# Performance work log

Hardware: AMD Instinct MI355X
Metric: run time of the kernel (lower is better)

Reference implementation:

```python
import jax, jax.numpy as jnp
import numpy as np

B, S, D = 1, 2048, 2048
H, KVH, HD = 32, 8, 64
FFN = 8192
N_EXPERTS, TOP_K = 32, 4
EPS = 1e-5
NEG = -1e9


def setup_inputs() -> dict:
    key = jax.random.key(0)
    ks = jax.random.split(key, 24)
    s = 0.02
    inp = {}
    inp['hidden_states'] = jax.random.normal(ks[0], (B, S, D), jnp.float32)
    # RoPE tables: cos/sin of shape [B, S, HD]
    inv_freq = 1.0 / (10000.0 ** (np.arange(0, HD, 2, dtype=np.float32) / HD))
    t = np.arange(S, dtype=np.float32)
    freqs = np.outer(t, inv_freq)                      # [S, HD/2]
    emb = np.concatenate([freqs, freqs], axis=-1)      # [S, HD]
    inp['cos'] = jnp.asarray(np.cos(emb))[None].repeat(B, axis=0)
    inp['sin'] = jnp.asarray(np.sin(emb))[None].repeat(B, axis=0)
    # additive causal mask [B, 1, S, S]
    causal = jnp.where(jnp.tril(jnp.ones((S, S), bool)), 0.0, NEG).astype(jnp.float32)
    inp['attention_mask'] = jnp.broadcast_to(causal[None, None], (B, 1, S, S))
    # attention params
    inp['wq'] = jax.random.normal(ks[1], (H * HD, D), jnp.float32) * s
    inp['bq'] = jnp.zeros((H * HD,), jnp.float32)
    inp['wk'] = jax.random.normal(ks[2], (KVH * HD, D), jnp.float32) * s
    inp['bk'] = jnp.zeros((KVH * HD,), jnp.float32)
    inp['wv'] = jax.random.normal(ks[3], (KVH * HD, D), jnp.float32) * s
    inp['bv'] = jnp.zeros((KVH * HD,), jnp.float32)
    inp['wo'] = jax.random.normal(ks[4], (D, H * HD), jnp.float32) * s
    inp['bo'] = jnp.zeros((D,), jnp.float32)
    # norms
    inp['ln1_w'] = jnp.ones((D,), jnp.float32)
    inp['ln2_w'] = jnp.ones((D,), jnp.float32)
    # MoE gate + shared expert MLP
    inp['gate_w'] = jax.random.normal(ks[5], (N_EXPERTS, D), jnp.float32) * s
    inp['gate_b'] = jnp.zeros((N_EXPERTS,), jnp.float32)
    inp['w1'] = jax.random.normal(ks[6], (FFN, D), jnp.float32) * s
    inp['b1'] = jnp.zeros((FFN,), jnp.float32)
    inp['w2'] = jax.random.normal(ks[7], (D, FFN), jnp.float32) * s
    inp['b2'] = jnp.zeros((D,), jnp.float32)
    inp['w3'] = jax.random.normal(ks[8], (FFN, D), jnp.float32) * s
    inp['b3'] = jnp.zeros((FFN,), jnp.float32)
    return inp


def _rms_norm(x, w, eps=EPS):
    x32 = x.astype(jnp.float32)
    var = jnp.mean(x32 * x32, axis=-1, keepdims=True)
    return (w * (x32 * jax.lax.rsqrt(var + eps))).astype(x.dtype)


def _rotate_half(x):
    x1, x2 = jnp.split(x, 2, axis=-1)
    return jnp.concatenate([-x2, x1], axis=-1)


def _decoder_layer(hidden_states, cos, sin, attention_mask,
                   wq, bq, wk, bk, wv, bv, wo, bo, ln1_w, ln2_w,
                   gate_w, gate_b, w1, b1, w2, b2, w3, b3):
    residual = hidden_states
    x = _rms_norm(hidden_states, ln1_w)

    # projections -> [B, heads, S, HD]
    q = (x @ wq.T + bq).reshape(B, S, H, HD).transpose(0, 2, 1, 3)
    k = (x @ wk.T + bk).reshape(B, S, KVH, HD).transpose(0, 2, 1, 3)
    v = (x @ wv.T + bv).reshape(B, S, KVH, HD).transpose(0, 2, 1, 3)

    # RoPE (cos/sin unsqueezed on head dim)
    c, s_ = cos[:, None], sin[:, None]
    q = q * c + _rotate_half(q) * s_
    k = k * c + _rotate_half(k) * s_

    # GQA: repeat kv heads
    n_rep = H // KVH
    k = jnp.repeat(k, n_rep, axis=1)
    v = jnp.repeat(v, n_rep, axis=1)

    scaling = HD ** -0.5
    scores = jnp.einsum('bhqd,bhkd->bhqk', q, k) * scaling + attention_mask
    probs = jax.nn.softmax(scores.astype(jnp.float32), axis=-1).astype(q.dtype)
    attn = jnp.einsum('bhqk,bhkd->bhqd', probs, v)
    attn = attn.transpose(0, 2, 1, 3).reshape(B, S, H * HD)
    attn = attn @ wo.T + bo

    hidden_states = residual + attn
    residual = hidden_states
    x = _rms_norm(hidden_states, ln2_w)

    # MoE block (as written in source: router computed, but ALL tokens go
    # through one shared expert MLP; routing weights unused in output)
    flat = x.reshape(-1, D)
    router_logits = flat @ gate_w.T + gate_b                     # [B*S, E]
    rw = jax.nn.softmax(router_logits.astype(jnp.float32), axis=-1)
    rw_top, sel = jax.lax.top_k(rw, TOP_K)                       # computed, unused
    del rw_top, sel

    h1 = flat @ w1.T + b1
    h3 = flat @ w3.T + b3
    mlp = (jax.nn.silu(h1) * h3) @ w2.T + b2
    hidden_states = residual + mlp.reshape(B, S, D)
    return hidden_states


def reference(hidden_states, cos, sin, attention_mask,
              wq, bq, wk, bk, wv, bv, wo, bo, ln1_w, ln2_w,
              gate_w, gate_b, w1, b1, w2, b2, w3, b3):
    return _decoder_layer(hidden_states, cos, sin, attention_mask,
                          wq, bq, wk, bk, wv, bv, wo, bo, ln1_w, ln2_w,
                          gate_w, gate_b, w1, b1, w2, b2, w3, b3)
```

## Files before the change

kernel.cpp:

```cpp
#include <hip/hip_runtime.h>

#define S_LEN 2048
#define DMODEL 2048
#define NH 32
#define NKV 8
#define HD 64
#define FFN_DIM 8192

typedef __attribute__((ext_vector_type(4))) float f32x4;
typedef __attribute__((ext_vector_type(16))) float f32x16;
typedef __attribute__((ext_vector_type(8))) short bf16x8;

#define MFMA(a, b, c) __builtin_amdgcn_mfma_f32_16x16x32_bf16(a, b, c, 0, 0, 0)
#define MFMA32(a, b, c) __builtin_amdgcn_mfma_f32_32x32x16_bf16(a, b, c, 0, 0, 0)

__device__ __forceinline__ ushort f2bf(float f) {
  unsigned u = __float_as_uint(f);
  unsigned r = (u + 0x7fffu + ((u >> 16) & 1u)) >> 16;
  return (ushort)r;
}
__device__ __forceinline__ float bf2f(ushort s) {
  return __uint_as_float(((unsigned)s) << 16);
}
__device__ __forceinline__ unsigned cvtpk(float a, float b) {
  unsigned r;
  asm("v_cvt_pk_bf16_f32 %0, %1, %2" : "=v"(r) : "v"(a), "v"(b));
  return r;
}

__device__ __forceinline__ void gload16(const void* g, void* l) {
  __builtin_amdgcn_global_load_lds(
      (const __attribute__((address_space(1))) void*)g,
      (__attribute__((address_space(3))) void*)l, 16, 0, 0);
}

__device__ __forceinline__ void cvt_row8(const float* src, ushort* dst,
                                         int i) {
  f32x4 a = *(const f32x4*)(src + i);
  f32x4 b = *(const f32x4*)(src + i + 4);
  bf16x8 r;
#pragma unroll
  for (int j = 0; j < 4; j++) r[j] = (short)f2bf(a[j]);
#pragma unroll
  for (int j = 0; j < 4; j++) r[4 + j] = (short)f2bf(b[j]);
  *(bf16x8*)(dst + i) = r;
}

__global__ __launch_bounds__(256) void pre_k(
    const float* __restrict__ hidden, const float* __restrict__ ln1,
    ushort* __restrict__ x1, const float* __restrict__ wq,
    const float* __restrict__ wk, const float* __restrict__ wv,
    ushort* __restrict__ cw, const float* __restrict__ bq,
    const float* __restrict__ bk, const float* __restrict__ bv,
    float* __restrict__ bqkv) {
  const int b = blockIdx.x;
  const int tid = threadIdx.x;
  if (b < 2048) {
    const float* x = hidden + (size_t)b * DMODEL;
    f32x4 v0 = *(const f32x4*)(x + tid * 8);
    f32x4 v1 = *(const f32x4*)(x + tid * 8 + 4);
    float ss = v0[0] * v0[0] + v0[1] * v0[1] + v0[2] * v0[2] + v0[3] * v0[3] +
               v1[0] * v1[0] + v1[1] * v1[1] + v1[2] * v1[2] + v1[3] * v1[3];
#pragma unroll
    for (int off = 32; off; off >>= 1) ss += __shfl_xor(ss, off, 64);
    __shared__ float red[4];
    if ((tid & 63) == 0) red[tid >> 6] = ss;
    __syncthreads();
    float tot = red[0] + red[1] + red[2] + red[3];
    float inv = rsqrtf(tot * (1.f / DMODEL) + 1e-5f);
#pragma unroll
    for (int i = 0; i < 8; i++) {
      int c = tid * 8 + i;
      float val = (i < 4) ? v0[i] : v1[i - 4];
      x1[(size_t)b * DMODEL + c] = f2bf(ln1[c] * val * inv);
    }
  } else if (b < 5120) {
    int row = b - 2048;
    const float* src;
    if (row < 2048) src = wq + (size_t)row * DMODEL;
    else if (row < 2560) src = wk + (size_t)(row - 2048) * DMODEL;
    else src = wv + (size_t)(row - 2560) * DMODEL;
    cvt_row8(src, cw + (size_t)row * DMODEL, tid * 8);
  } else {
    int i = (b - 5120) * 256 + tid;
    float v;
    if (i < 2048) v = bq[i];
    else if (i < 2560) v = bk[i - 2048];
    else v = bv[i - 2560];
    bqkv[i] = v;
  }
}

__global__ __launch_bounds__(256) void cvt_k(const float* __restrict__ in,
                                             ushort* __restrict__ out) {
  int i = blockIdx.x * 256 + threadIdx.x;
  f32x4 a = ((const f32x4*)in)[i * 2];
  f32x4 b = ((const f32x4*)in)[i * 2 + 1];
  bf16x8 r;
#pragma unroll
  for (int j = 0; j < 4; j++) r[j] = (short)f2bf(a[j]);
#pragma unroll
  for (int j = 0; j < 4; j++) r[4 + j] = (short)f2bf(b[j]);
  ((bf16x8*)out)[i] = r;
}

__global__ __launch_bounds__(256) void cvt_w13_k(const float* __restrict__ w1,
                                                 const float* __restrict__ w3,
                                                 ushort* __restrict__ dst) {
  int r = blockIdx.x;
  int nb = r >> 8, i5 = r & 255;
  int wn = i5 >> 6, nf = (i5 >> 4) & 3, e = i5 & 15;
  int L = nb * 128 + wn * 32 + (nf >> 1) * 16 + e;
  const float* src = ((nf & 1) ? w3 : w1) + (size_t)L * DMODEL;
  cvt_row8(src, dst + (size_t)r * DMODEL, threadIdx.x * 8);
}

enum { EPI_PART = 0, EPI_SILU2 = 1 };

#define QUAD(AS, BS, MROW, NCOL)                                     \
  _Pragma("unroll") for (int kk_ = 0; kk_ < 2; kk_++)                \
  _Pragma("unroll") for (int mf_ = 0; mf_ < 4; mf_++)                \
  _Pragma("unroll") for (int nf_ = 0; nf_ < 2; nf_++)                \
      acc[(MROW) + mf_][(NCOL) + nf_] =                              \
          MFMA(AS[2 * mf_ + kk_], BS[2 * nf_ + kk_],                 \
               acc[(MROW) + mf_][(NCOL) + nf_]);

#define PHASE_MID                                    \
  __builtin_amdgcn_sched_barrier(0);                 \
  __builtin_amdgcn_s_barrier();                      \
  asm volatile("s_waitcnt lgkmcnt(0)" ::: "memory"); \
  __builtin_amdgcn_sched_barrier(0);                 \
  __builtin_amdgcn_s_setprio(1);

#define PHASE_CLOSE                                  \
  __builtin_amdgcn_s_setprio(0);                     \
  __builtin_amdgcn_sched_barrier(0);                 \
  __builtin_amdgcn_s_barrier();

#define RD_A(PA0, PA1, J0)                           \
  _Pragma("unroll") for (int j_ = 0; j_ < 4; j_++) { \
    A_[2 * j_] = *(const bf16x8*)((PA0) + ((J0) + j_) * 1024);     \
    A_[2 * j_ + 1] = *(const bf16x8*)((PA1) + ((J0) + j_) * 1024); \
  }
#define RD_B(DST, PB0, PB1, J0)                      \
  _Pragma("unroll") for (int n_ = 0; n_ < 2; n_++) { \
    DST[2 * n_] = *(const bf16x8*)((PB0) + ((J0) + n_) * 1024);     \
    DST[2 * n_ + 1] = *(const bf16x8*)((PB1) + ((J0) + n_) * 1024); \
  }

template <int EPI>
__global__ __launch_bounds__(512, 2) void gemm256(
    const ushort* __restrict__ A, int lda, const ushort* __restrict__ B,
    int ldb, const float* __restrict__ b1v, const float* __restrict__ b3v,
    ushort* __restrict__ outb, int ldc, int K, int kspan, long long opart) {
  __shared__ __align__(16) ushort lds[65536];
  const int tid = threadIdx.x;
  const int l = tid & 63, w = tid >> 6;
  const int g = l >> 4, r16 = l & 15;
  const int wm = w >> 2, wn = w & 3;

  int nwg = gridDim.x * gridDim.y;
  int bid = blockIdx.y * gridDim.x + blockIdx.x;
  bid = (bid & 7) * (nwg >> 3) + (bid >> 3);
  const int m0 = (bid % gridDim.x) * 256;
  const int n0 = (bid / gridDim.x) * 256;
  const int z = blockIdx.z;

  const ushort* Ag = A + (size_t)z * kspan + (size_t)m0 * lda;
  const ushort* Bg = B + (size_t)z * kspan + (size_t)n0 * ldb;
  ushort* outbz = outb + (size_t)z * opart;

  const int NT = K >> 6, NI = NT >> 1;

  const int stgRow = w * 8 + (l >> 3);
  const int stgCol = ((l & 7) ^ (l >> 3)) * 8;

  const int xa = (r16 & 7) << 4;
  const int c0 = ((g * 16) ^ xa) >> 1;
  const int c1 = c0 ^ 32;
  const int aslot = wm ? 24576 : 8192;
  const int bslot = ((wn >> 1) ? 16384 : 0) + (wn & 1) * 4096;
  const ushort* pA0b0 = lds + aslot + r16 * 64 + c0;
  const ushort* pA1b0 = lds + aslot + r16 * 64 + c1;
  const ushort* pA0b1 = pA0b0 + 32768;
  const ushort* pA1b1 = pA1b0 + 32768;
  const ushort* pB0b0 = lds + bslot + r16 * 64 + c0;
  const ushort* pB1b0 = lds + bslot + r16 * 64 + c1;
  const ushort* pB0b1 = pB0b0 + 32768;
  const ushort* pB1b1 = pB1b0 + 32768;

  f32x4 acc[8][4];
#pragma unroll
  for (int i = 0; i < 8; i++)
#pragma unroll
    for (int j = 0; j < 4; j++) acc[i][j] = (f32x4){0, 0, 0, 0};

  auto stageA = [&](int slot, int tile, int hf) {
    ushort* dst = lds + ((tile & 1) * 32768 + slot * 8192 + w * 512);
    const ushort* src =
        Ag + (size_t)(hf * 128 + stgRow) * lda + tile * 64 + stgCol;
    gload16(src, dst);
    gload16(src + (size_t)64 * lda, dst + 4096);
  };
  auto stageB = [&](int slot, int tile, int hf) {
    ushort* dst = lds + ((tile & 1) * 32768 + slot * 8192 + w * 512);
    const ushort* src =
        Bg + (size_t)(hf * 128 + stgRow) * ldb + tile * 64 + stgCol;
    gload16(src, dst);
    gload16(src + (size_t)64 * ldb, dst + 4096);
  };

  stageB(0, 0, 0);
  stageB(2, 0, 1);
  stageA(1, 0, 0);
  stageA(3, 0, 1);
  stageB(0, 1, 0);
  stageB(2, 1, 1);
  asm volatile("s_waitcnt vmcnt(4)" ::: "memory");
  __builtin_amdgcn_s_barrier();

  bf16x8 A_[8], Blo[4], Bhi[4];

  for (int i = 0; i < NI; ++i) {
    const int ta = 2 * i, tb = 2 * i + 1;
    const bool st = (ta + 2 < NT);
    RD_A(pA0b0, pA1b0, 0);
    RD_B(Blo, pB0b0, pB1b0, 0);
    stageA(1, tb, 0);
    asm volatile("s_waitcnt lgkmcnt(8)" ::: "memory");
    PHASE_MID; QUAD(A_, Blo, 0, 0); PHASE_CLOSE;
    RD_B(Bhi, pB0b0, pB1b0, 2);
    stageA(3, tb, 1);
    PHASE_MID; QUAD(A_, Bhi, 0, 2); PHASE_CLOSE;
    RD_A(pA0b0, pA1b0, 4);
    if (st) stageB(0, ta + 2, 0);
    PHASE_MID; QUAD(A_, Bhi, 4, 2); PHASE_CLOSE;
    if (st) stageB(2, ta + 2, 1);
    PHASE_MID; QUAD(A_, Blo, 4, 0);
    __builtin_amdgcn_s_setprio(0);
    __builtin_amdgcn_sched_barrier(0);
    if (st) {
      asm volatile("s_waitcnt vmcnt(4)" ::: "memory");
    } else {
      asm volatile("s_waitcnt vmcnt(0)" ::: "memory");
    }
    __builtin_amdgcn_s_barrier();
    RD_A(pA0b1, pA1b1, 0);
    RD_B(Blo, pB0b1, pB1b1, 0);
    if (st) stageA(1, ta + 2, 0);
    asm volatile("s_waitcnt lgkmcnt(8)" ::: "memory");
    PHASE_MID; QUAD(A_, Blo, 0, 0); PHASE_CLOSE;
    RD_B(Bhi, pB0b1, pB1b1, 2);
    if (st) stageA(3, ta + 2, 1);
    PHASE_MID; QUAD(A_, Bhi, 0, 2); PHASE_CLOSE;
    RD_A(pA0b1, pA1b1, 4);
    if (st) stageB(0, tb + 2, 0);
    PHASE_MID; QUAD(A_, Bhi, 4, 2); PHASE_CLOSE;
    if (st) stageB(2, tb + 2, 1);
    PHASE_MID; QUAD(A_, Blo, 4, 0);
    __builtin_amdgcn_s_setprio(0);
    __builtin_amdgcn_sched_barrier(0);
    asm volatile("s_waitcnt vmcnt(4)" ::: "memory");
    __builtin_amdgcn_s_barrier();
  }

  if constexpr (EPI == EPI_PART) {
#pragma unroll
    for (int mf = 0; mf < 8; mf++)
#pragma unroll
      for (int nf = 0; nf < 4; nf++) {
        const int n = n0 + wn * 64 + nf * 16 + r16;
#pragma unroll
        for (int reg = 0; reg < 4; reg++) {
          const int m = m0 + wm * 128 + mf * 16 + g * 4 + reg;
          outbz[(size_t)m * ldc + n] = f2bf(acc[mf][nf][reg]);
        }
      }
  } else {
#pragma unroll
    for (int mf = 0; mf < 8; mf++)
#pragma unroll
      for (int p = 0; p < 2; p++) {
        const int L = (n0 >> 1) + wn * 32 + p * 16 + r16;
        const float bb1 = b1v[L], bb3 = b3v[L];
#pragma unroll
        for (int reg = 0; reg < 4; reg++) {
          const int m = m0 + wm * 128 + mf * 16 + g * 4 + reg;
          float h1 = acc[mf][2 * p][reg] + bb1;
          float h3 = acc[mf][2 * p + 1][reg] + bb3;
          float sv = h1 / (1.f + __expf(-h1));
          outbz[(size_t)m * ldc + L] = f2bf(sv * h3);
        }
      }
  }
}

__global__ __launch_bounds__(384) void reduceQ_rope_k(
    const ushort* __restrict__ part, const float* __restrict__ bias,
    const float* __restrict__ cs, const float* __restrict__ sn,
    ushort* __restrict__ qkv) {
  __shared__ float row[3072];
  const int r = blockIdx.x;
  const int col = threadIdx.x * 8;
  const long long ps = (long long)S_LEN * 3072;
  float s[8];
#pragma unroll
  for (int j = 0; j < 8; j++) s[j] = bias[col + j];
#pragma unroll
  for (int z = 0; z < 2; z++) {
    bf16x8 v = *(const bf16x8*)(part + z * ps + (size_t)r * 3072 + col);
#pragma unroll
    for (int j = 0; j < 8; j++) s[j] += bf2f((ushort)v[j]);
  }
#pragma unroll
  for (int j = 0; j < 8; j++) row[col + j] = s[j];
  __syncthreads();
  ushort o[8];
  if (col < 2560) {
    const float* c = cs + r * HD + (col & 63);
    const float* si = sn + r * HD + (col & 63);
    const float sgn = (col & 32) ? 1.f : -1.f;
    const int pc = col ^ 32;
#pragma unroll
    for (int j = 0; j < 8; j++)
      o[j] = f2bf(s[j] * c[j] + sgn * row[pc + j] * si[j]);
  } else {
#pragma unroll
    for (int j = 0; j < 8; j++) o[j] = f2bf(s[j]);
  }
  bf16x8 rr;
#pragma unroll
  for (int j = 0; j < 8; j++) rr[j] = (short)o[j];
  *(bf16x8*)(qkv + (size_t)r * 3072 + col) = rr;
}

__global__ __launch_bounds__(256) void reduceO_rms_k(
    const ushort* __restrict__ part, const float* __restrict__ bias,
    const float* __restrict__ resid, const float* __restrict__ lnw,
    float* __restrict__ outf, ushort* __restrict__ x2) {
  const int r = blockIdx.x;
  const int tid = threadIdx.x;
  const int col = tid * 8;
  const long long ps = (long long)S_LEN * DMODEL;
  float s[8];
#pragma unroll
  for (int j = 0; j < 8; j++) s[j] = bias[col + j] + resid[(size_t)r * DMODEL + col + j];
#pragma unroll
  for (int z = 0; z < 4; z++) {
    bf16x8 v = *(const bf16x8*)(part + z * ps + (size_t)r * DMODEL + col);
#pragma unroll
    for (int j = 0; j < 8; j++) s[j] += bf2f((ushort)v[j]);
  }
  float ss = 0.f;
#pragma unroll
  for (int j = 0; j < 8; j++) ss += s[j] * s[j];
#pragma unroll
  for (int off = 32; off; off >>= 1) ss += __shfl_xor(ss, off, 64);
  __shared__ float red[4];
  if ((tid & 63) == 0) red[tid >> 6] = ss;
  f32x4 o0, o1;
#pragma unroll
  for (int j = 0; j < 4; j++) { o0[j] = s[j]; o1[j] = s[4 + j]; }
  *(f32x4*)(outf + (size_t)r * DMODEL + col) = o0;
  *(f32x4*)(outf + (size_t)r * DMODEL + col + 4) = o1;
  __syncthreads();
  float tot = red[0] + red[1] + red[2] + red[3];
  float inv = rsqrtf(tot * (1.f / DMODEL) + 1e-5f);
  bf16x8 rr;
#pragma unroll
  for (int j = 0; j < 8; j++) rr[j] = (short)f2bf(lnw[col + j] * s[j] * inv);
  *(bf16x8*)(x2 + (size_t)r * DMODEL + col) = rr;
}

__global__ __launch_bounds__(256) void reduceW_k(
    const ushort* __restrict__ part, const float* __restrict__ bias,
    float* __restrict__ out) {
  long long i = (long long)(blockIdx.x * 256 + threadIdx.x) * 8;
  int col = (int)(i % DMODEL);
  const long long ps = (long long)S_LEN * DMODEL;
  float s[8];
#pragma unroll
  for (int j = 0; j < 8; j++) s[j] = bias[col + j] + out[i + j];
#pragma unroll
  for (int z = 0; z < 4; z++) {
    bf16x8 v = *(const bf16x8*)(part + z * ps + i);
#pragma unroll
    for (int j = 0; j < 8; j++) s[j] += bf2f((ushort)v[j]);
  }
#pragma unroll
  for (int j = 0; j < 8; j++) out[i + j] = s[j];
}

__global__ __launch_bounds__(128, 3) void flash2_k(
    const ushort* __restrict__ qkv, ushort* __restrict__ att, int nFlash,
    int nCvtTasks, const float* __restrict__ wo, const float* __restrict__ w1,
    const float* __restrict__ w3, const float* __restrict__ w2s,
    ushort* __restrict__ cwA, ushort* __restrict__ cwB) {
  if ((int)blockIdx.x >= nFlash) {
    const int cb = blockIdx.x - nFlash;
    const int NC = gridDim.x - nFlash;
    const int i = threadIdx.x * 8;
    for (int t = cb; t < nCvtTasks; t += NC) {
      const float* src;
      ushort* dst;
      if (t < 2048) {
        src = wo + (size_t)t * DMODEL;
        dst = cwB + (size_t)t * DMODEL;
      } else if (t < 18432) {
        int r = t - 2048;
        int nb = r >> 8, i5 = r & 255;
        int wn = i5 >> 6, nf = (i5 >> 4) & 3, e = i5 & 15;
        int L = nb * 128 + wn * 32 + (nf >> 1) * 16 + e;
        src = ((nf & 1) ? w3 : w1) + (size_t)L * DMODEL;
        dst = cwA + (size_t)r * DMODEL;
      } else {
        int r = t - 18432;
        src = w2s + (size_t)r * 2048;
        dst = cwB + (size_t)2048 * DMODEL + (size_t)r * 2048;
      }
      cvt_row8(src, dst, i);
      cvt_row8(src, dst, i + 1024);
    }
    return;
  }
  const int bid = blockIdx.x;
  const int head = (bid >> 5) & 31;
  const int rmap = bid & 31;
  const int qb = (bid & 512) ? (31 - rmap) : rmap;
  const int kvh = head >> 2;
  const int tid = threadIdx.x;
  const int w = tid >> 6, l = tid & 63;
  const int h = l >> 5, q31 = l & 31;
  const int qw = qb * 64 + w * 32;
  const int qrow = qw + q31;

  __shared__ __align__(16) ushort lds[2][8192];

  bf16x8 qreg[4];
  {
    const ushort* qp = qkv + (size_t)qrow * 3072 + head * HD;
#pragma unroll
    for (int s = 0; s < 4; s++)
      qreg[s] = *(const bf16x8*)(qp + s * 16 + h * 8);
  }

  f32x16 oacc[2];
#pragma unroll
  for (int i = 0; i < 16; i++) { oacc[0][i] = 0.f; oacc[1][i] = 0.f; }
  float mreg = -1e30f, lsum = 0.f;

  const int nt = qb + 1;

  const int skv = tid >> 1;
  const int sc4 = (tid & 1) * 4;
  const int vkv = tid & 63;
  const int vd0 = (tid >> 6) * 32;

  const ushort* kg_base = qkv + DMODEL + kvh * HD;

  bf16x8 kr[4], vr[4];
  auto loadTile = [&](int jb) {
    const ushort* kg = kg_base + (size_t)jb * 64 * 3072;
#pragma unroll
    for (int c = 0; c < 4; c++)
      kr[c] = *(const bf16x8*)(kg + (size_t)skv * 3072 + (sc4 + c) * 8);
    const ushort* vg = kg + 512;
#pragma unroll
    for (int c = 0; c < 4; c++)
      vr[c] = *(const bf16x8*)(vg + (size_t)vkv * 3072 + vd0 + c * 8);
  };
  auto writeTile = [&](int b) {
    ushort* kb = lds[b];
#pragma unroll
    for (int c = 0; c < 4; c++)
      *(bf16x8*)(kb + skv * 64 + (((sc4 + c) ^ (skv & 7)) * 8)) = kr[c];
    ushort* vb = lds[b] + 4096;
#pragma unroll
    for (int c = 0; c < 4; c++)
#pragma unroll
      for (int i = 0; i < 8; i++) {
        int d = vd0 + c * 8 + i;
        vb[d * 64 + (((vkv >> 3) ^ (d & 7)) * 8) + (vkv & 7)] = (ushort)vr[c][i];
      }
  };

  loadTile(0);
  for (int jb = 0; jb < nt; ++jb) {
    const int b = jb & 1;
    writeTile(b);
    __syncthreads();
    if (jb + 1 < nt) loadTile(jb + 1);

    if (jb * 64 <= qw + 31) {
      const ushort* Kb = lds[b];
      const ushort* Vb = lds[b] + 4096;

      f32x16 sacc[2];
#pragma unroll
      for (int i = 0; i < 16; i++) { sacc[0][i] = 0.f; sacc[1][i] = 0.f; }
#pragma unroll
      for (int c = 0; c < 2; c++) {
        const int kvr = c * 32 + q31;
        const ushort* kp = Kb + kvr * 64;
        const int kx = kvr & 7;
#pragma unroll
        for (int s = 0; s < 4; s++) {
          bf16x8 kf = *(const bf16x8*)(kp + ((2 * s + h) ^ kx) * 8);
          sacc[c] = MFMA32(kf, qreg[s], sacc[c]);
        }
      }

      const bool diag = (jb * 64 + 63 > qw);
      if (diag) {
#pragma unroll
        for (int c = 0; c < 2; c++)
#pragma unroll
          for (int rg = 0; rg < 16; rg++) {
            int kvg = jb * 64 + c * 32 + (rg & 3) + 8 * (rg >> 2) + 4 * h;
            if (kvg > qrow) sacc[c][rg] = -1e30f;
          }
      }
      float tmax = sacc[0][0];
#pragma unroll
      for (int rg = 1; rg < 16; rg++) tmax = fmaxf(tmax, sacc[0][rg]);
#pragma unroll
      for (int rg = 0; rg < 16; rg++) tmax = fmaxf(tmax, sacc[1][rg]);
      tmax = fmaxf(tmax, __shfl_xor(tmax, 32));
      const float mn = fmaxf(mreg, tmax);
      const float resc = __expf((mreg - mn) * 0.125f);
      mreg = mn;
      float rsum = 0.f;
#pragma unroll
      for (int c = 0; c < 2; c++)
#pragma unroll
        for (int rg = 0; rg < 16; rg++) {
          float pv = __expf((sacc[c][rg] - mn) * 0.125f);
          sacc[c][rg] = pv;
          rsum += pv;
        }
      rsum += __shfl_xor(rsum, 32);
      lsum = lsum * resc + rsum;
      oacc[0] *= resc;
      oacc[1] *= resc;

      unsigned pw_[2][4][2];
#pragma unroll
      for (int c = 0; c < 2; c++)
#pragma unroll
        for (int rr = 0; rr < 4; rr++) {
          pw_[c][rr][0] = cvtpk(sacc[c][4 * rr + 0], sacc[c][4 * rr + 1]);
          pw_[c][rr][1] = cvtpk(sacc[c][4 * rr + 2], sacc[c][4 * rr + 3]);
        }

#pragma unroll
      for (int s = 0; s < 4; s++) {
        const int c = s >> 1, base = (s & 1) * 2;
        unsigned k0 = h ? pw_[c][base + 1][0] : pw_[c][base][0];
        unsigned k1 = h ? pw_[c][base + 1][1] : pw_[c][base][1];
        unsigned s0 = h ? pw_[c][base][0] : pw_[c][base + 1][0];
        unsigned s1 = h ? pw_[c][base][1] : pw_[c][base + 1][1];
        unsigned t0 = __shfl_xor(s0, 32);
        unsigned t1 = __shfl_xor(s1, 32);
        union { unsigned u[4]; bf16x8 v; } pf;
        pf.u[0] = h ? t0 : k0;
        pf.u[1] = h ? t1 : k1;
        pf.u[2] = h ? k0 : t0;
        pf.u[3] = h ? k1 : t1;
#pragma unroll
        for (int dt = 0; dt < 2; dt++) {
          const int d = dt * 32 + q31;
          bf16x8 vf =
              *(const bf16x8*)(Vb + d * 64 + ((2 * s + h) ^ (d & 7)) * 8);
          oacc[dt] = MFMA32(vf, pf.v, oacc[dt]);
        }
      }
    }
  }

  const float inv = 1.f / lsum;
  ushort* op = att + (size_t)qrow * DMODEL + head * HD;
#pragma unroll
  for (int dt = 0; dt < 2; dt++)
#pragma unroll
    for (int rr = 0; rr < 4; rr++) {
      const int d0 = dt * 32 + 8 * rr + 4 * h;
      unsigned lo = cvtpk(oacc[dt][4 * rr + 0] * inv, oacc[dt][4 * rr + 1] * inv);
      unsigned hi = cvtpk(oacc[dt][4 * rr + 2] * inv, oacc[dt][4 * rr + 3] * inv);
      uint2 v2;
      v2.x = lo;
      v2.y = hi;
      *(uint2*)(op + d0) = v2;
    }
}

extern "C" void kernel_launch(void* const* d_in, const int* in_sizes, int n_in,
                              void* d_out, int out_size, void* d_ws,
                              size_t ws_size, hipStream_t stream) {
  (void)in_sizes; (void)n_in; (void)out_size;
  const float* hidden = (const float*)d_in[0];
  const float* cosb = (const float*)d_in[1];
  const float* sinb = (const float*)d_in[2];
  const float* wq = (const float*)d_in[4];
  const float* bq = (const float*)d_in[5];
  const float* wk = (const float*)d_in[6];
  const float* bk = (const float*)d_in[7];
  const float* wv = (const float*)d_in[8];
  const float* bv = (const float*)d_in[9];
  const float* wo = (const float*)d_in[10];
  const float* bo = (const float*)d_in[11];
  const float* ln1 = (const float*)d_in[12];
  const float* ln2 = (const float*)d_in[13];
  const float* w1 = (const float*)d_in[16];
  const float* b1 = (const float*)d_in[17];
  const float* w2 = (const float*)d_in[18];
  const float* b2 = (const float*)d_in[19];
  const float* w3 = (const float*)d_in[20];
  const float* b3 = (const float*)d_in[21];
  float* out = (float*)d_out;

  char* base = (char*)d_ws;
  char* ws = base;
  ushort* x1 = (ushort*)ws;   ws += (size_t)S_LEN * DMODEL * 2;
  ushort* qkv = (ushort*)ws;  ws += (size_t)S_LEN * 3072 * 2;
  ushort* att = (ushort*)ws;  ws += (size_t)S_LEN * DMODEL * 2;
  ushort* x2 = (ushort*)ws;   ws += (size_t)S_LEN * DMODEL * 2;
  ushort* hbuf = (ushort*)ws; ws += (size_t)S_LEN * FFN_DIM * 2;
  ushort* cwA = (ushort*)ws;  ws += (size_t)2 * FFN_DIM * DMODEL * 2;
  float* bqkv = (float*)ws;   ws += 4096 * 4;
  ushort* cwB = (ushort*)ws;
  const size_t cwB_bytes = (size_t)(2048 + 8192) * DMODEL * 2;
  const bool bigws = ((size_t)(ws - base) + cwB_bytes) <= ws_size;

  ushort* partQ = att;
  ushort* partO = hbuf;
  ushort* partW = x1;

  pre_k<<<5132, 256, 0, stream>>>(hidden, ln1, x1, wq, wk, wv, cwA, bq, bk, bv,
                                  bqkv);

  gemm256<EPI_PART><<<dim3(8, 12, 2), 512, 0, stream>>>(
      x1, DMODEL, cwA, DMODEL, nullptr, nullptr, partQ, 3072, 1024, 1024,
      (long long)S_LEN * 3072);
  reduceQ_rope_k<<<S_LEN, 384, 0, stream>>>(partQ, bqkv, cosb, sinb, qkv);

  const ushort *Bo, *B13, *B2;
  if (bigws) {
    flash2_k<<<1024 + 512, 128, 0, stream>>>(qkv, att, 1024, 26624, wo, w1, w3,
                                             w2, cwA, cwB);
    Bo = cwB;
    B13 = cwA;
    B2 = cwB + (size_t)2048 * DMODEL;
  } else {
    flash2_k<<<1024, 128, 0, stream>>>(qkv, att, 1024, 0, wo, w1, w3, w2, cwA,
                                       cwA);
    Bo = cwA;
    B13 = cwA;
    B2 = cwA;
  }

  if (!bigws) cvt_k<<<(2048 * 2048) / 2048, 256, 0, stream>>>(wo, (ushort*)Bo);
  gemm256<EPI_PART><<<dim3(8, 8, 4), 512, 0, stream>>>(
      att, DMODEL, Bo, DMODEL, nullptr, nullptr, partO, DMODEL, 512, 512,
      (long long)S_LEN * DMODEL);
  reduceO_rms_k<<<S_LEN, 256, 0, stream>>>(partO, bo, hidden, ln2, out, x2);

  if (!bigws) cvt_w13_k<<<2 * FFN_DIM, 256, 0, stream>>>(w1, w3, (ushort*)B13);
  gemm256<EPI_SILU2><<<dim3(8, 64), 512, 0, stream>>>(
      x2, DMODEL, B13, DMODEL, b1, b3, hbuf, FFN_DIM, DMODEL, 0, 0);

  if (!bigws) cvt_k<<<(DMODEL * FFN_DIM) / 2048, 256, 0, stream>>>(w2, (ushort*)B2);
  gemm256<EPI_PART><<<dim3(8, 8, 4), 512, 0, stream>>>(
      hbuf, FFN_DIM, B2, FFN_DIM, nullptr, nullptr, partW, DMODEL, 2048, 2048,
      (long long)S_LEN * DMODEL);
  reduceW_k<<<(S_LEN * DMODEL) / 2048, 256, 0, stream>>>(partW, b2, out);
}
```

Baseline: 377.0 us.

## Replace split-K 256-tile GEMMs with simple 128-tile GEMM for QKV, O, W2

Adds a simple 128x128-tile bf16 MFMA GEMM without software pipelining and uses it for the QKV, output-projection and W2 GEMMs. Split-K is removed for QKV and O and halved for W2, so the reduction kernels read fewer partial buffers. The goal is less partial-sum traffic and more blocks per GEMM. In exchange the new GEMM has no double buffering and lower per-block reuse than the tuned 256 kernel, so load latency may be exposed.

Measured after the change: 431.6 us. 1.14x slower.

```diff
diff --git a/kernel.cpp b/kernel.cpp
--- a/kernel.cpp
+++ b/kernel.cpp
@@ -113,6 +113,89 @@
   int L = nb * 128 + wn * 32 + (nf >> 1) * 16 + e;
   const float* src = ((nf & 1) ? w3 : w1) + (size_t)L * DMODEL;
   cvt_row8(src, dst + (size_t)r * DMODEL, threadIdx.x * 8);
+}
+
+__global__ __launch_bounds__(256) void gemm128(
+    const ushort* __restrict__ A, int lda, const ushort* __restrict__ B,
+    int ldb, ushort* __restrict__ outb, int ldc, int K, int kspan,
+    long long opart) {
+  __shared__ __align__(16) ushort lds[16384];
+  const int tid = threadIdx.x;
+  const int l = tid & 63, w = tid >> 6;
+  const int g = l >> 4, r16 = l & 15;
+  const int wm = w >> 1, wn = w & 1;
+
+  int nwg = gridDim.x * gridDim.y;
+  int bid = blockIdx.y * gridDim.x + blockIdx.x;
+  bid = (bid & 7) * (nwg >> 3) + (bid >> 3);
+  const int m0 = (bid % gridDim.x) * 128;
+  const int n0 = (bid / gridDim.x) * 128;
+  const int z = blockIdx.z;
+
+  const ushort* Ag = A + (size_t)z * kspan + (size_t)m0 * lda;
+  const ushort* Bg = B + (size_t)z * kspan + (size_t)n0 * ldb;
+  ushort* outbz = outb + (size_t)z * opart;
+
+  const int NT = K >> 6;
+
+  const int stgRow = w * 8 + (l >> 3);
+  const int stgCol = ((l & 7) ^ (l >> 3)) * 8;
+  const int xa = (r16 & 7) << 4;
+  const int c0 = ((g * 16) ^ xa) >> 1;
+  const int c1 = c0 ^ 32;
+  const ushort* pA0 = lds + (wm * 64 + r16) * 64 + c0;
+  const ushort* pA1 = lds + (wm * 64 + r16) * 64 + c1;
+  const ushort* pB0 = lds + 8192 + (wn * 64 + r16) * 64 + c0;
+  const ushort* pB1 = lds + 8192 + (wn * 64 + r16) * 64 + c1;
+
+  f32x4 acc[4][4];
+#pragma unroll
+  for (int i = 0; i < 4; i++)
+#pragma unroll
+    for (int j = 0; j < 4; j++) acc[i][j] = (f32x4){0, 0, 0, 0};
+
+  for (int t = 0; t < NT; ++t) {
+#pragma unroll
+    for (int p = 0; p < 4; p++) {
+      const int row = p * 32 + stgRow;
+      gload16(Ag + (size_t)row * lda + t * 64 + stgCol,
+              lds + (p * 32 + w * 8) * 64);
+      gload16(Bg + (size_t)row * ldb + t * 64 + stgCol,
+              lds + 8192 + (p * 32 + w * 8) * 64);
+    }
+    __syncthreads();
+    bf16x8 Ar[8], Br[8];
+#pragma unroll
+    for (int mt = 0; mt < 4; mt++) {
+      Ar[2 * mt] = *(const bf16x8*)(pA0 + mt * 1024);
+      Ar[2 * mt + 1] = *(const bf16x8*)(pA1 + mt * 1024);
+    }
+#pragma unroll
+    for (int nt = 0; nt < 4; nt++) {
+      Br[2 * nt] = *(const bf16x8*)(pB0 + nt * 1024);
+      Br[2 * nt + 1] = *(const bf16x8*)(pB1 + nt * 1024);
+    }
+#pragma unroll
+    for (int kk = 0; kk < 2; kk++)
+#pragma unroll
+      for (int mt = 0; mt < 4; mt++)
+#pragma unroll
+        for (int nt = 0; nt < 4; nt++)
+          acc[mt][nt] = MFMA(Ar[2 * mt + kk], Br[2 * nt + kk], acc[mt][nt]);
+    __syncthreads();
+  }
+
+#pragma unroll
+  for (int mf = 0; mf < 4; mf++)
+#pragma unroll
+    for (int nf = 0; nf < 4; nf++) {
+      const int n = n0 + wn * 64 + nf * 16 + r16;
+#pragma unroll
+      for (int reg = 0; reg < 4; reg++) {
+        const int m = m0 + wm * 64 + mf * 16 + g * 4 + reg;
+        outbz[(size_t)m * ldc + n] = f2bf(acc[mf][nf][reg]);
+      }
+    }
 }
 
 enum { EPI_PART = 0, EPI_SILU2 = 1 };
@@ -295,6 +378,7 @@
   }
 }
 
+template <int NZ>
 __global__ __launch_bounds__(384) void reduceQ_rope_k(
     const ushort* __restrict__ part, const float* __restrict__ bias,
     const float* __restrict__ cs, const float* __restrict__ sn,
@@ -307,7 +391,7 @@
 #pragma unroll
   for (int j = 0; j < 8; j++) s[j] = bias[col + j];
 #pragma unroll
-  for (int z = 0; z < 2; z++) {
+  for (int z = 0; z < NZ; z++) {
     bf16x8 v = *(const bf16x8*)(part + z * ps + (size_t)r * 3072 + col);
 #pragma unroll
     for (int j = 0; j < 8; j++) s[j] += bf2f((ushort)v[j]);
@@ -334,6 +418,7 @@
   *(bf16x8*)(qkv + (size_t)r * 3072 + col) = rr;
 }
 
+template <int NZ>
 __global__ __launch_bounds__(256) void reduceO_rms_k(
     const ushort* __restrict__ part, const float* __restrict__ bias,
     const float* __restrict__ resid, const float* __restrict__ lnw,
@@ -346,7 +431,7 @@
 #pragma unroll
   for (int j = 0; j < 8; j++) s[j] = bias[col + j] + resid[(size_t)r * DMODEL + col + j];
 #pragma unroll
-  for (int z = 0; z < 4; z++) {
+  for (int z = 0; z < NZ; z++) {
     bf16x8 v = *(const bf16x8*)(part + z * ps + (size_t)r * DMODEL + col);
 #pragma unroll
     for (int j = 0; j < 8; j++) s[j] += bf2f((ushort)v[j]);
@@ -372,6 +457,7 @@
   *(bf16x8*)(x2 + (size_t)r * DMODEL + col) = rr;
 }
 
+template <int NZ>
 __global__ __launch_bounds__(256) void reduceW_k(
     const ushort* __restrict__ part, const float* __restrict__ bias,
     float* __restrict__ out) {
@@ -382,7 +468,7 @@
 #pragma unroll
   for (int j = 0; j < 8; j++) s[j] = bias[col + j] + out[i + j];
 #pragma unroll
-  for (int z = 0; z < 4; z++) {
+  for (int z = 0; z < NZ; z++) {
     bf16x8 v = *(const bf16x8*)(part + z * ps + i);
 #pragma unroll
     for (int j = 0; j < 8; j++) s[j] += bf2f((ushort)v[j]);
@@ -638,10 +724,9 @@
   pre_k<<<5132, 256, 0, stream>>>(hidden, ln1, x1, wq, wk, wv, cwA, bq, bk, bv,
                                   bqkv);
 
-  gemm256<EPI_PART><<<dim3(8, 12, 2), 512, 0, stream>>>(
-      x1, DMODEL, cwA, DMODEL, nullptr, nullptr, partQ, 3072, 1024, 1024,
-      (long long)S_LEN * 3072);
-  reduceQ_rope_k<<<S_LEN, 384, 0, stream>>>(partQ, bqkv, cosb, sinb, qkv);
+  gemm128<<<dim3(16, 24), 256, 0, stream>>>(x1, DMODEL, cwA, DMODEL, partQ,
+                                            3072, DMODEL, 0, 0);
+  reduceQ_rope_k<1><<<S_LEN, 384, 0, stream>>>(partQ, bqkv, cosb, sinb, qkv);
 
   const ushort *Bo, *B13, *B2;
   if (bigws) {
@@ -659,18 +744,17 @@
   }
 
   if (!bigws) cvt_k<<<(2048 * 2048) / 2048, 256, 0, stream>>>(wo, (ushort*)Bo);
-  gemm256<EPI_PART><<<dim3(8, 8, 4), 512, 0, stream>>>(
-      att, DMODEL, Bo, DMODEL, nullptr, nullptr, partO, DMODEL, 512, 512,
-      (long long)S_LEN * DMODEL);
-  reduceO_rms_k<<<S_LEN, 256, 0, stream>>>(partO, bo, hidden, ln2, out, x2);
+  gemm128<<<dim3(16, 16), 256, 0, stream>>>(att, DMODEL, Bo, DMODEL, partO,
+                                            DMODEL, DMODEL, 0, 0);
+  reduceO_rms_k<1><<<S_LEN, 256, 0, stream>>>(partO, bo, hidden, ln2, out, x2);
 
   if (!bigws) cvt_w13_k<<<2 * FFN_DIM, 256, 0, stream>>>(w1, w3, (ushort*)B13);
   gemm256<EPI_SILU2><<<dim3(8, 64), 512, 0, stream>>>(
       x2, DMODEL, B13, DMODEL, b1, b3, hbuf, FFN_DIM, DMODEL, 0, 0);
 
   if (!bigws) cvt_k<<<(DMODEL * FFN_DIM) / 2048, 256, 0, stream>>>(w2, (ushort*)B2);
-  gemm256<EPI_PART><<<dim3(8, 8, 4), 512, 0, stream>>>(
-      hbuf, FFN_DIM, B2, FFN_DIM, nullptr, nullptr, partW, DMODEL, 2048, 2048,
-      (long long)S_LEN * DMODEL);
-  reduceW_k<<<(S_LEN * DMODEL) / 2048, 256, 0, stream>>>(partW, b2, out);
-}
+  gemm128<<<dim3(16, 16, 2), 256, 0, stream>>>(hbuf, FFN_DIM, B2, FFN_DIM,
+                                               partW, DMODEL, 4096, 4096,
+                                               (long long)S_LEN * DMODEL);
+  reduceW_k<2><<<(S_LEN * DMODEL) / 2048, 256, 0, stream>>>(partW, b2, out);
+}
```
